# Kernel tuning notes

Hardware: AMD Instinct MI355X
Metric: run time of the kernel (lower is better)

Reference implementation:

```python
import jax, jax.numpy as jnp
import numpy as np

N = 50000
E = 100000
H = 768          # hidden_size
NH = 12          # num_heads
HD = H // NH     # head dim = 64
NG = 64          # number of graphs in batch
NC = 10          # num_classes
NEG_SLOPE = 0.2


def _p(key, shape, scale=0.05):
    return jax.random.normal(key, shape, dtype=jnp.float32) * scale


def setup_inputs() -> dict:
    key = jax.random.key(0)
    ks = jax.random.split(key, 24)
    x = jax.random.normal(ks[0], (N, 3), dtype=jnp.float32)
    edge_index = jax.random.randint(ks[1], (2, E), 0, N, dtype=jnp.int32)
    batch = jnp.sort(jax.random.randint(ks[2], (N,), 0, NG, dtype=jnp.int32))
    inp = {
        'x': x, 'edge_index': edge_index, 'batch': batch,
        # GCN layers
        'w1': _p(ks[3], (3, H)), 'b1': jnp.zeros((H,), jnp.float32),
        'w2': _p(ks[4], (H, H)), 'b2': jnp.zeros((H,), jnp.float32),
        'w3': _p(ks[5], (H, H)), 'b3': jnp.zeros((H,), jnp.float32),
        # GAT layer 1
        'wg1': _p(ks[6], (H, H)), 'as1': _p(ks[7], (NH, HD)), 'ad1': _p(ks[8], (NH, HD)), 'bg1': jnp.zeros((H,), jnp.float32),
        # GAT layer 2
        'wg2': _p(ks[9], (H, H)), 'as2': _p(ks[10], (NH, HD)), 'ad2': _p(ks[11], (NH, HD)), 'bg2': jnp.zeros((H,), jnp.float32),
        # classifier MLP
        'wc1': _p(ks[12], (H, H // 2)), 'bc1': jnp.zeros((H // 2,), jnp.float32),
        'wc2': _p(ks[13], (H // 2, NC)), 'bc2': jnp.zeros((NC,), jnp.float32),
    }
    return inp


def _add_self_loops(edge_index):
    loop = jnp.arange(N, dtype=edge_index.dtype)
    src = jnp.concatenate([edge_index[0], loop])
    dst = jnp.concatenate([edge_index[1], loop])
    return src, dst


def gcn_conv(x, w, b, src, dst):
    # PyG GCNConv: self-loops + symmetric normalization D^-1/2 A D^-1/2
    h = x @ w                                   # [N, out]
    deg = jnp.zeros((N,), h.dtype).at[dst].add(1.0)   # includes self-loops -> >= 1
    dinv = jax.lax.rsqrt(deg)
    norm = (dinv[src] * dinv[dst])[:, None]     # [E', 1]
    msg = h[src] * norm                          # gather-scale
    out = jnp.zeros_like(h).at[dst].add(msg)     # scatter-add
    return out + b


def gat_conv(x, w, a_src, a_dst, b, src, dst):
    # PyG GATConv: self-loops, LeakyReLU(0.2), scatter-softmax over dst, concat heads
    h = (x @ w).reshape(N, NH, HD)
    alpha_s = jnp.einsum('nhd,hd->nh', h, a_src)  # [N, H]
    alpha_d = jnp.einsum('nhd,hd->nh', h, a_dst)
    e = jax.nn.leaky_relu(alpha_s[src] + alpha_d[dst], NEG_SLOPE)  # [E', H]
    m = jax.ops.segment_max(e, dst, num_segments=N)                 # [N, H]
    ex = jnp.exp(e - m[dst])
    s = jax.ops.segment_sum(ex, dst, num_segments=N)
    alpha = ex / s[dst]                                             # [E', H]
    out = jax.ops.segment_sum(h[src] * alpha[:, :, None], dst, num_segments=N)
    return out.reshape(N, NH * HD) + b


def global_mean_pool(x, batch):
    s = jax.ops.segment_sum(x, batch, num_segments=NG)
    cnt = jax.ops.segment_sum(jnp.ones((N,), x.dtype), batch, num_segments=NG)
    return s / jnp.maximum(cnt, 1.0)[:, None]


def reference(x, edge_index, batch, w1, b1, w2, b2, w3, b3,
              wg1, as1, ad1, bg1, wg2, as2, ad2, bg2,
              wc1, bc1, wc2, bc2):
    src, dst = _add_self_loops(edge_index)
    h = jax.nn.relu(gcn_conv(x, w1, b1, src, dst))
    # dropout is identity in eval mode
    h = jax.nn.relu(gcn_conv(h, w2, b2, src, dst))
    h = jax.nn.relu(gcn_conv(h, w3, b3, src, dst))
    h = jax.nn.relu(gat_conv(h, wg1, as1, ad1, bg1, src, dst))
    h = gat_conv(h, wg2, as2, ad2, bg2, src, dst)
    g = global_mean_pool(h, batch)                 # [NG, H]
    z = jax.nn.relu(g @ wc1 + bc1)
    logits = z @ wc2 + bc2                         # [NG, NC]
    return logits
```

## Files before the change

### kernel.cpp

```cpp
#include <hip/hip_runtime.h>
#include <math.h>

#define N_NODES 50000
#define N_EDGES 100000
#define H 768
#define NH 12
#define HD 64
#define NG 64
#define NC 10
#define H2 384
#define PCH 32
#define NSB 196

typedef _Float16 h8  __attribute__((ext_vector_type(8)));
typedef _Float16 h4v __attribute__((ext_vector_type(4)));
typedef float    ffrag __attribute__((ext_vector_type(4)));

__device__ _Float16 g_ah[(size_t)N_NODES * H];
__device__ _Float16 g_ch[(size_t)N_NODES * H];
__device__ _Float16 g_wh[4 * H * H];
__device__ float    g_dinv[N_NODES];
__device__ int      g_degi[N_NODES];
__device__ int      g_bsum[256];
__device__ int      g_boff[256];
__device__ int      g_cursor[N_NODES];
__device__ int      g_rowptr[N_NODES + 1];
__device__ int      g_csrsrc[N_EDGES];
__device__ float    g_aS[(size_t)N_NODES * NH];
__device__ float    g_aD[(size_t)N_NODES * NH];
__device__ float    g_selfc[(size_t)N_NODES * NH];
__device__ float    g_coef[(size_t)N_EDGES * NH];
__device__ float    g_ppool[(size_t)NG * PCH * H];

__device__ inline int clampi(int v, int hi) { return (v < 0) ? 0 : (v >= hi ? hi - 1 : v); }

__device__ inline void gload_lds16(const _Float16* g, _Float16* s) {
    __builtin_amdgcn_global_load_lds(
        (const __attribute__((address_space(1))) void*)g,
        (__attribute__((address_space(3))) void*)s, 16, 0, 0);
}

__global__ void fill_i32(int* p, int n, int v) {
    int i = blockIdx.x * blockDim.x + threadIdx.x;
    if (i < n) p[i] = v;
}

__global__ void count_deg(const int* __restrict__ dst, int* __restrict__ degi) {
    int e = blockIdx.x * blockDim.x + threadIdx.x;
    if (e < N_EDGES) atomicAdd(&degi[clampi(dst[e], N_NODES)], 1);
}

__global__ __launch_bounds__(256) void scan1(const int* __restrict__ degi, int* __restrict__ bsum) {
    __shared__ int s[256];
    int b = blockIdx.x, t = threadIdx.x;
    int idx = b * 256 + t;
    s[t] = (idx < N_NODES) ? degi[idx] : 0;
    __syncthreads();
    for (int off = 128; off > 0; off >>= 1) {
        if (t < off) s[t] += s[t + off];
        __syncthreads();
    }
    if (t == 0) bsum[b] = s[0];
}

__global__ __launch_bounds__(256) void scan2(const int* __restrict__ bsum, int* __restrict__ boff,
                                             int* __restrict__ rowptr) {
    __shared__ int s[256];
    int t = threadIdx.x;
    int v = (t < NSB) ? bsum[t] : 0;
    s[t] = v;
    __syncthreads();
    for (int off = 1; off < 256; off <<= 1) {
        int x = (t >= off) ? s[t - off] : 0;
        __syncthreads();
        s[t] += x;
        __syncthreads();
    }
    if (t < NSB) boff[t] = s[t] - v;
    if (t == NSB - 1) rowptr[N_NODES] = s[t];
}

__global__ __launch_bounds__(256) void scan3(const int* __restrict__ degi, const int* __restrict__ boff,
                                             int* __restrict__ rowptr, int* __restrict__ cursor,
                                             float* __restrict__ dinv) {
    __shared__ int s[256];
    int b = blockIdx.x, t = threadIdx.x;
    int idx = b * 256 + t;
    int v = (idx < N_NODES) ? degi[idx] : 0;
    s[t] = v;
    __syncthreads();
    for (int off = 1; off < 256; off <<= 1) {
        int x = (t >= off) ? s[t - off] : 0;
        __syncthreads();
        s[t] += x;
        __syncthreads();
    }
    if (idx < N_NODES) {
        int excl = s[t] - v + boff[b];
        rowptr[idx] = excl;
        cursor[idx] = excl;
        dinv[idx] = rsqrtf((float)v + 1.0f);
    }
}

__global__ void bin_edges(const int* __restrict__ src, const int* __restrict__ dst,
                          int* __restrict__ cursor, int* __restrict__ csrsrc) {
    int e = blockIdx.x * blockDim.x + threadIdx.x;
    if (e >= N_EDGES) return;
    int d = clampi(dst[e], N_NODES);
    int pos = atomicAdd(&cursor[d], 1);
    if (pos >= 0 && pos < N_EDGES) csrsrc[pos] = clampi(src[e], N_NODES);
}

__global__ void split_wT4(const float* __restrict__ w2, const float* __restrict__ w3,
                          const float* __restrict__ wg1, const float* __restrict__ wg2,
                          _Float16* __restrict__ out) {
    int idx = blockIdx.x * blockDim.x + threadIdx.x;
    if (idx >= 4 * H * H) return;
    int l = idx / (H * H), r = idx % (H * H);
    const float* w = (l == 0) ? w2 : (l == 1) ? w3 : (l == 2) ? wg1 : wg2;
    int n = r % H, k = r / H;
    out[(size_t)l * H * H + (size_t)n * H + k] = (_Float16)w[(size_t)k * H + n];
}

__global__ void gcn1_fused(const int* __restrict__ rowptr, const int* __restrict__ csrsrc,
                           const float* __restrict__ x, const float* __restrict__ dinv,
                           const float* __restrict__ w1, const float* __restrict__ b1,
                           _Float16* __restrict__ hi) {
    int d = blockIdx.x * 2 + (threadIdx.x / 96);
    int t = threadIdx.x % 96;
    if (d >= N_NODES) return;
    float dd = dinv[d];
    float c = dd * dd;
    float s0 = x[d*3] * c, s1 = x[d*3+1] * c, s2 = x[d*3+2] * c;
    int beg = rowptr[d], end = rowptr[d + 1];
    for (int i = beg; i < end; i++) {
        int s = csrsrc[i];
        float cc = dinv[s] * dd;
        s0 += x[s*3] * cc; s1 += x[s*3+1] * cc; s2 += x[s*3+2] * cc;
    }
    int j0 = t * 8;
    h8 o;
    #pragma unroll
    for (int k = 0; k < 8; k++) {
        int j = j0 + k;
        float v = s0 * w1[j] + s1 * w1[H + j] + s2 * w1[2*H + j] + b1[j];
        o[k] = (_Float16)fmaxf(v, 0.f);
    }
    ((h8*)(hi + (size_t)d * H))[t] = o;
}

__global__ __launch_bounds__(512) void gemm_f16(const _Float16* __restrict__ a,
                                                const _Float16* __restrict__ bt,
                                                _Float16* __restrict__ C, int M,
                                                const float* __restrict__ asf,
                                                const float* __restrict__ adf,
                                                float* __restrict__ aS,
                                                float* __restrict__ aD) {
    __shared__ _Float16 sA[2][2][128 * 32], sB[2][2][128 * 32];
    int tid = threadIdx.x;
    int wave = tid >> 6, lane = tid & 63;
    int quad = lane >> 4, l16 = lane & 15;

    int id = blockIdx.x;
    int x = id & 7;
    int s = id >> 3;
    int strip = x + 8 * (s / 6);
    int colt = s % 6;
    if (strip >= (N_NODES + 127) / 128) return;
    int row0 = strip * 128, col0 = colt * 128;
    int wr = (wave >> 1) * 32, wc = (wave & 1) * 64;

    int rr = lane >> 2;
    int kc = (((lane & 3) ^ ((lane >> 3) & 3)) << 3);
    const _Float16* gptr[4];
    int sel[4];
    int soff[4];
    #pragma unroll
    for (int k = 0; k < 4; k++) {
        int sg = wave * 4 + k;
        int isA = (sg < 16);
        int s2 = sg & 15;
        int khalf = s2 >> 3, rowgroup = s2 & 7;
        int r = (isA ? row0 : col0) + rowgroup * 16 + rr;
        if (isA && r >= M) r = M - 1;
        gptr[k] = (isA ? a : bt) + (size_t)r * H + khalf * 32 + kc;
        sel[k] = isA ? 0 : 1;
        soff[k] = khalf * 4096 + rowgroup * 512;
    }

    int fsw = (quad ^ ((l16 >> 1) & 3)) * 8;

    ffrag acc[2][4];
    #pragma unroll
    for (int i = 0; i < 2; i++)
        #pragma unroll
        for (int j = 0; j < 4; j++) { ffrag z = {0.f, 0.f, 0.f, 0.f}; acc[i][j] = z; }

    #pragma unroll
    for (int k = 0; k < 4; k++)
        gload_lds16(gptr[k], (sel[k] ? &sB[0][0][0] : &sA[0][0][0]) + soff[k]);

    #pragma unroll 1
    for (int kt = 0; kt < H / 64; kt++) {
        int cur = kt & 1;
        __syncthreads();
        if (kt + 1 < H / 64) {
            int koff = (kt + 1) * 64;
            #pragma unroll
            for (int k = 0; k < 4; k++)
                gload_lds16(gptr[k] + koff,
                            (sel[k] ? &sB[cur ^ 1][0][0] : &sA[cur ^ 1][0][0]) + soff[k]);
        }

        #pragma unroll
        for (int kk = 0; kk < 2; kk++) {
            const _Float16* pA = sA[cur][kk];
            const _Float16* pB = sB[cur][kk];
            h8 fa[2], fb[4];
            #pragma unroll
            for (int i = 0; i < 2; i++)
                fa[i] = *reinterpret_cast<const h8*>(&pA[(wr + i * 16 + l16) * 32 + fsw]);
            #pragma unroll
            for (int j = 0; j < 4; j++)
                fb[j] = *reinterpret_cast<const h8*>(&pB[(wc + j * 16 + l16) * 32 + fsw]);
            #pragma unroll
            for (int i = 0; i < 2; i++)
                #pragma unroll
                for (int j = 0; j < 4; j++)
                    acc[i][j] = __builtin_amdgcn_mfma_f32_16x16x32_f16(fa[i], fb[j], acc[i][j], 0, 0, 0);
        }
    }

    #pragma unroll
    for (int i = 0; i < 2; i++)
        #pragma unroll
        for (int r = 0; r < 4; r++) {
            int row = row0 + wr + i * 16 + quad * 4 + r;
            if (row >= M) continue;
            #pragma unroll
            for (int j = 0; j < 4; j++)
                C[(size_t)row * H + col0 + wc + j * 16 + l16] = (_Float16)acc[i][j][r];
        }

    if (asf) {
        int head = (col0 + wc) >> 6;
        float as_c[4], ad_c[4];
        #pragma unroll
        for (int j = 0; j < 4; j++) {
            int col = col0 + wc + j * 16 + l16;
            as_c[j] = asf[col];
            ad_c[j] = adf[col];
        }
        #pragma unroll
        for (int i = 0; i < 2; i++)
            #pragma unroll
            for (int r = 0; r < 4; r++) {
                float ps = 0.f, pd = 0.f;
                #pragma unroll
                for (int j = 0; j < 4; j++) {
                    ps += acc[i][j][r] * as_c[j];
                    pd += acc[i][j][r] * ad_c[j];
                }
                ps += __shfl_xor(ps, 1);  pd += __shfl_xor(pd, 1);
                ps += __shfl_xor(ps, 2);  pd += __shfl_xor(pd, 2);
                ps += __shfl_xor(ps, 4);  pd += __shfl_xor(pd, 4);
                ps += __shfl_xor(ps, 8);  pd += __shfl_xor(pd, 8);
                int row = row0 + wr + i * 16 + quad * 4 + r;
                if (l16 == 0 && row < M) {
                    aS[row * NH + head] = ps;
                    aD[row * NH + head] = pd;
                }
            }
    }
}

__global__ void gcn_gather(const int* __restrict__ rowptr, const int* __restrict__ csrsrc,
                           const _Float16* __restrict__ h, const float* __restrict__ dinv,
                           const float* __restrict__ bias, _Float16* __restrict__ hi) {
    int d = blockIdx.x * 2 + (threadIdx.x / 96);
    int t = threadIdx.x % 96;
    if (d >= N_NODES) return;
    float dd = dinv[d];
    float c = dd * dd;
    h8 v = ((const h8*)(h + (size_t)d * H))[t];
    float acc[8];
    #pragma unroll
    for (int k = 0; k < 8; k++) acc[k] = (float)v[k] * c;
    int beg = rowptr[d], end = rowptr[d + 1];
    for (int i = beg; i < end; i++) {
        int s = csrsrc[i];
        float cc = dinv[s] * dd;
        h8 u = ((const h8*)(h + (size_t)s * H))[t];
        #pragma unroll
        for (int k = 0; k < 8; k++) acc[k] += (float)u[k] * cc;
    }
    float4 b0 = ((const float4*)bias)[2 * t];
    float4 b1 = ((const float4*)bias)[2 * t + 1];
    h8 o;
    o[0] = (_Float16)fmaxf(acc[0] + b0.x, 0.f);
    o[1] = (_Float16)fmaxf(acc[1] + b0.y, 0.f);
    o[2] = (_Float16)fmaxf(acc[2] + b0.z, 0.f);
    o[3] = (_Float16)fmaxf(acc[3] + b0.w, 0.f);
    o[4] = (_Float16)fmaxf(acc[4] + b1.x, 0.f);
    o[5] = (_Float16)fmaxf(acc[5] + b1.y, 0.f);
    o[6] = (_Float16)fmaxf(acc[6] + b1.z, 0.f);
    o[7] = (_Float16)fmaxf(acc[7] + b1.w, 0.f);
    ((h8*)(hi + (size_t)d * H))[t] = o;
}

__device__ inline float lrelu(float v) { return (v > 0.f) ? v : 0.2f * v; }

__global__ void gat_stats(const int* __restrict__ rowptr, const int* __restrict__ csrsrc,
                          const float* __restrict__ aS, const float* __restrict__ aD,
                          float* __restrict__ selfc, float* __restrict__ coef) {
    int idx = blockIdx.x * blockDim.x + threadIdx.x;
    if (idx >= N_NODES * NH) return;
    int d = idx / NH, hh = idx % NH;
    int beg = rowptr[d], end = rowptr[d + 1];
    float adv = aD[idx];
    float eself = lrelu(aS[idx] + adv);
    float m = eself;
    for (int i = beg; i < end; i++)
        m = fmaxf(m, lrelu(aS[csrsrc[i] * NH + hh] + adv));
    float ssum = __expf(eself - m);
    for (int i = beg; i < end; i++)
        ssum += __expf(lrelu(aS[csrsrc[i] * NH + hh] + adv) - m);
    float inv = 1.0f / ssum;
    selfc[idx] = __expf(eself - m) * inv;
    for (int i = beg; i < end; i++)
        coef[(size_t)i * NH + hh] = __expf(lrelu(aS[csrsrc[i] * NH + hh] + adv) - m) * inv;
}

__global__ void gat_gather(const int* __restrict__ rowptr, const int* __restrict__ csrsrc,
                           const _Float16* __restrict__ h, const float* __restrict__ selfc,
                           const float* __restrict__ coef, const float* __restrict__ bias,
                           _Float16* __restrict__ hi, int relu) {
    int d = blockIdx.x * 2 + (threadIdx.x / 96);
    int t = threadIdx.x % 96;
    if (d >= N_NODES) return;
    int hh = t >> 3;
    int beg = rowptr[d], end = rowptr[d + 1];
    float cself = selfc[d * NH + hh];
    h8 v = ((const h8*)(h + (size_t)d * H))[t];
    float acc[8];
    #pragma unroll
    for (int k = 0; k < 8; k++) acc[k] = (float)v[k] * cself;
    for (int i = beg; i < end; i++) {
        int s = csrsrc[i];
        float c = coef[(size_t)i * NH + hh];
        h8 u = ((const h8*)(h + (size_t)s * H))[t];
        #pragma unroll
        for (int k = 0; k < 8; k++) acc[k] += (float)u[k] * c;
    }
    float4 b0 = ((const float4*)bias)[2 * t];
    float4 b1 = ((const float4*)bias)[2 * t + 1];
    acc[0] += b0.x; acc[1] += b0.y; acc[2] += b0.z; acc[3] += b0.w;
    acc[4] += b1.x; acc[5] += b1.y; acc[6] += b1.z; acc[7] += b1.w;
    if (relu) {
        #pragma unroll
        for (int k = 0; k < 8; k++) acc[k] = fmaxf(acc[k], 0.f);
    }
    h8 o;
    #pragma unroll
    for (int k = 0; k < 8; k++) o[k] = (_Float16)acc[k];
    ((h8*)(hi + (size_t)d * H))[t] = o;
}

__device__ inline int lower_bound_i(const int* b, int n, int key) {
    int lo = 0, hi = n;
    while (lo < hi) { int mid = (lo + hi) >> 1; if (b[mid] < key) lo = mid + 1; else hi = mid; }
    return lo;
}

__global__ void pool_partial(const int* __restrict__ batch, const _Float16* __restrict__ h,
                             float* __restrict__ ppool) {
    int g = blockIdx.x / PCH, c = blockIdx.x % PCH;
    int t = threadIdx.x;
    int lo = lower_bound_i(batch, N_NODES, g);
    int hi = lower_bound_i(batch, N_NODES, g + 1);
    int len = hi - lo;
    int chunk = (len + PCH - 1) / PCH;
    int s = lo + c * chunk;
    int e = s + chunk; if (e > hi) e = hi;
    float4 a = {0, 0, 0, 0};
    for (int n = s; n < e; n++) {
        h4v v = ((const h4v*)(h + (size_t)n * H))[t];
        a.x += (float)v[0]; a.y += (float)v[1]; a.z += (float)v[2]; a.w += (float)v[3];
    }
    ((float4*)(ppool + (size_t)blockIdx.x * H))[t] = a;
}

__global__ __launch_bounds__(384) void pool_mlp(const int* __restrict__ batch,
                                                const float* __restrict__ ppool,
                                                const float* __restrict__ wc1,
                                                const float* __restrict__ bc1,
                                                const float* __restrict__ wc2,
                                                const float* __restrict__ bc2,
                                                float* __restrict__ out) {
    __shared__ float row[H];
    __shared__ float z[H2];
    int g = blockIdx.x, t = threadIdx.x;
    int lo = lower_bound_i(batch, N_NODES, g);
    int hi = lower_bound_i(batch, N_NODES, g + 1);
    float inv = 1.0f / fmaxf((float)(hi - lo), 1.0f);
    for (int c0 = t; c0 < H; c0 += 384) {
        float a = 0.f;
        for (int c = 0; c < PCH; c++) a += ppool[(size_t)(g * PCH + c) * H + c0];
        row[c0] = a * inv;
    }
    __syncthreads();
    float acc = bc1[t];
    for (int k = 0; k < H; k++) acc += row[k] * wc1[(size_t)k * H2 + t];
    z[t] = fmaxf(acc, 0.f);
    __syncthreads();
    if (t < NC) {
        float l = bc2[t];
        for (int k = 0; k < H2; k++) l += z[k] * wc2[(size_t)k * NC + t];
        out[g * NC + t] = l;
    }
}

extern "C" void kernel_launch(void* const* d_in, const int* in_sizes, int n_in,
                              void* d_out, int out_size, void* d_ws, size_t ws_size,
                              hipStream_t stream) {
    (void)d_ws; (void)ws_size;
    const float* x     = (const float*)d_in[0];
    const int*   ei    = (const int*)d_in[1];
    const int*   batch = (const int*)d_in[2];
    const float* w1  = (const float*)d_in[3];  const float* b1  = (const float*)d_in[4];
    const float* w2  = (const float*)d_in[5];  const float* b2  = (const float*)d_in[6];
    const float* w3  = (const float*)d_in[7];  const float* b3  = (const float*)d_in[8];
    const float* wg1 = (const float*)d_in[9];  const float* as1 = (const float*)d_in[10];
    const float* ad1 = (const float*)d_in[11]; const float* bg1 = (const float*)d_in[12];
    const float* wg2 = (const float*)d_in[13]; const float* as2 = (const float*)d_in[14];
    const float* ad2 = (const float*)d_in[15]; const float* bg2 = (const float*)d_in[16];
    const float* wc1 = (const float*)d_in[17]; const float* bc1 = (const float*)d_in[18];
    const float* wc2 = (const float*)d_in[19]; const float* bc2 = (const float*)d_in[20];

    const int* srcp = ei;
    const int* dstp = ei + N_EDGES;

    float *dinv, *aS, *aD, *selfc, *coef, *ppool;
    _Float16 *ah, *ch, *wh;
    int *degi, *bsum, *boff, *cursor, *rowptr, *csrsrc;
    hipGetSymbolAddress((void**)&ah,     HIP_SYMBOL(g_ah));
    hipGetSymbolAddress((void**)&ch,     HIP_SYMBOL(g_ch));
    hipGetSymbolAddress((void**)&wh,     HIP_SYMBOL(g_wh));
    hipGetSymbolAddress((void**)&dinv,   HIP_SYMBOL(g_dinv));
    hipGetSymbolAddress((void**)&degi,   HIP_SYMBOL(g_degi));
    hipGetSymbolAddress((void**)&bsum,   HIP_SYMBOL(g_bsum));
    hipGetSymbolAddress((void**)&boff,   HIP_SYMBOL(g_boff));
    hipGetSymbolAddress((void**)&cursor, HIP_SYMBOL(g_cursor));
    hipGetSymbolAddress((void**)&rowptr, HIP_SYMBOL(g_rowptr));
    hipGetSymbolAddress((void**)&csrsrc, HIP_SYMBOL(g_csrsrc));
    hipGetSymbolAddress((void**)&aS,     HIP_SYMBOL(g_aS));
    hipGetSymbolAddress((void**)&aD,     HIP_SYMBOL(g_aD));
    hipGetSymbolAddress((void**)&selfc,  HIP_SYMBOL(g_selfc));
    hipGetSymbolAddress((void**)&coef,   HIP_SYMBOL(g_coef));
    hipGetSymbolAddress((void**)&ppool,  HIP_SYMBOL(g_ppool));

    auto cdiv = [](int a, int b) { return (a + b - 1) / b; };
    int ggrid = 8 * cdiv(cdiv(N_NODES, 128), 8) * (H / 128);
    int ngath = cdiv(N_NODES, 2);
    size_t HH = (size_t)H * H;

    split_wT4<<<cdiv(4*H*H,256),256,0,stream>>>(w2, w3, wg1, wg2, wh);

    fill_i32<<<cdiv(N_NODES,256),256,0,stream>>>(degi, N_NODES, 0);
    count_deg<<<cdiv(N_EDGES,256),256,0,stream>>>(dstp, degi);
    scan1<<<NSB,256,0,stream>>>(degi, bsum);
    scan2<<<1,256,0,stream>>>(bsum, boff, rowptr);
    scan3<<<NSB,256,0,stream>>>(degi, boff, rowptr, cursor, dinv);
    bin_edges<<<cdiv(N_EDGES,256),256,0,stream>>>(srcp, dstp, cursor, csrsrc);

    gcn1_fused<<<ngath,192,0,stream>>>(rowptr, csrsrc, x, dinv, w1, b1, ah);

    gemm_f16<<<ggrid,512,0,stream>>>(ah, wh + 0*HH, ch, N_NODES,
                                     (const float*)nullptr, (const float*)nullptr,
                                     (float*)nullptr, (float*)nullptr);
    gcn_gather<<<ngath,192,0,stream>>>(rowptr, csrsrc, ch, dinv, b2, ah);

    gemm_f16<<<ggrid,512,0,stream>>>(ah, wh + 1*HH, ch, N_NODES,
                                     (const float*)nullptr, (const float*)nullptr,
                                     (float*)nullptr, (float*)nullptr);
    gcn_gather<<<ngath,192,0,stream>>>(rowptr, csrsrc, ch, dinv, b3, ah);

    gemm_f16<<<ggrid,512,0,stream>>>(ah, wh + 2*HH, ch, N_NODES, as1, ad1, aS, aD);
    gat_stats<<<cdiv(N_NODES*NH,256),256,0,stream>>>(rowptr, csrsrc, aS, aD, selfc, coef);
    gat_gather<<<ngath,192,0,stream>>>(rowptr, csrsrc, ch, selfc, coef, bg1, ah, 1);

    gemm_f16<<<ggrid,512,0,stream>>>(ah, wh + 3*HH, ch, N_NODES, as2, ad2, aS, aD);
    gat_stats<<<cdiv(N_NODES*NH,256),256,0,stream>>>(rowptr, csrsrc, aS, aD, selfc, coef);
    gat_gather<<<ngath,192,0,stream>>>(rowptr, csrsrc, ch, selfc, coef, bg2, ah, 0);

    pool_partial<<<NG*PCH,192,0,stream>>>(batch, ah, ppool);
    pool_mlp<<<NG,384,0,stream>>>(batch, ppool, wc1, bc1, wc2, bc2, (float*)d_out);
}
```

Baseline: 819.1 us.

## Enlarge GEMM tile to 256x128 with triple-buffered LDS pipeline and XCD remap

The f16 MFMA GEMM now uses a 256x128 output tile per block, so each wave computes 64x64 instead of 32x64. The K loop keeps three 64-wide LDS buffers and prefetches two steps ahead, with explicit vmcnt/lgkmcnt waits and raw barriers instead of __syncthreads. It raises MFMA priority during compute and remaps block ids round-robin over 8 groups of 147 (likely per-XCD). The aim is more reuse per loaded tile and better hiding of global load latency, at the cost of more accumulator registers and 144KB of LDS per block, which limits occupancy.

```diff
diff --git a/kernel.cpp b/kernel.cpp
--- a/kernel.cpp
+++ b/kernel.cpp
@@ -157,103 +157,151 @@
                                                 const float* __restrict__ adf,
                                                 float* __restrict__ aS,
                                                 float* __restrict__ aD) {
-    __shared__ _Float16 sA[2][2][128 * 32], sB[2][2][128 * 32];
+    __shared__ alignas(16) _Float16 lds[3][24576];
+
     int tid = threadIdx.x;
     int wave = tid >> 6, lane = tid & 63;
     int quad = lane >> 4, l16 = lane & 15;
-
-    int id = blockIdx.x;
-    int x = id & 7;
-    int s = id >> 3;
-    int strip = x + 8 * (s / 6);
-    int colt = s % 6;
-    if (strip >= (N_NODES + 127) / 128) return;
-    int row0 = strip * 128, col0 = colt * 128;
-    int wr = (wave >> 1) * 32, wc = (wave & 1) * 64;
-
-    int rr = lane >> 2;
-    int kc = (((lane & 3) ^ ((lane >> 3) & 3)) << 3);
-    const _Float16* gptr[4];
-    int sel[4];
-    int soff[4];
-    #pragma unroll
-    for (int k = 0; k < 4; k++) {
-        int sg = wave * 4 + k;
-        int isA = (sg < 16);
-        int s2 = sg & 15;
-        int khalf = s2 >> 3, rowgroup = s2 & 7;
-        int r = (isA ? row0 : col0) + rowgroup * 16 + rr;
-        if (isA && r >= M) r = M - 1;
-        gptr[k] = (isA ? a : bt) + (size_t)r * H + khalf * 32 + kc;
-        sel[k] = isA ? 0 : 1;
-        soff[k] = khalf * 4096 + rowgroup * 512;
-    }
-
-    int fsw = (quad ^ ((l16 >> 1) & 3)) * 8;
-
-    ffrag acc[2][4];
-    #pragma unroll
-    for (int i = 0; i < 2; i++)
+    int wm = wave >> 1, wn = wave & 1;
+
+    int orig = blockIdx.x;
+    int wgid = (orig & 7) * 147 + (orig >> 3);
+    int strip = wgid / 6, colt = wgid % 6;
+    int row0 = strip * 256, col0 = colt * 128;
+
+    int lr = lane >> 3;
+    int lc = lane & 7;
+    int cg = lc ^ lr;
+    const _Float16* gA[4];
+    const _Float16* gB[2];
+    int stA[4], stB[2];
+    #pragma unroll
+    for (int g = 0; g < 4; g++) {
+        int rA = row0 + wave * 32 + g * 8 + lr;
+        if (rA >= M) rA = M - 1;
+        gA[g] = a + (size_t)rA * H + cg * 8;
+        stA[g] = (wave * 32 + g * 8) * 64;
+    }
+    #pragma unroll
+    for (int g = 0; g < 2; g++) {
+        int rB = col0 + wave * 16 + g * 8 + lr;
+        gB[g] = bt + (size_t)rB * H + cg * 8;
+        stB[g] = 16384 + (wave * 16 + g * 8) * 64;
+    }
+
+    int swz = l16 & 7;
+    int offA[4][2], offB[4][2];
+    #pragma unroll
+    for (int i = 0; i < 4; i++)
+        #pragma unroll
+        for (int kk = 0; kk < 2; kk++) {
+            offA[i][kk] = (wm * 64 + i * 16 + l16) * 64 + (((kk * 4 + quad) ^ swz) * 8);
+            offB[i][kk] = 16384 + (wn * 64 + i * 16 + l16) * 64 + (((kk * 4 + quad) ^ swz) * 8);
+        }
+
+    ffrag acc[4][4];
+    #pragma unroll
+    for (int i = 0; i < 4; i++)
         #pragma unroll
         for (int j = 0; j < 4; j++) { ffrag z = {0.f, 0.f, 0.f, 0.f}; acc[i][j] = z; }
 
-    #pragma unroll
-    for (int k = 0; k < 4; k++)
-        gload_lds16(gptr[k], (sel[k] ? &sB[0][0][0] : &sA[0][0][0]) + soff[k]);
-
+    _Float16* p0 = &lds[0][0];
+    _Float16* p1 = &lds[1][0];
+    _Float16* p2 = &lds[2][0];
+
+    #pragma unroll
+    for (int g = 0; g < 4; g++) gload_lds16(gA[g], p0 + stA[g]);
+    #pragma unroll
+    for (int g = 0; g < 2; g++) gload_lds16(gB[g], p0 + stB[g]);
+    #pragma unroll
+    for (int g = 0; g < 4; g++) gload_lds16(gA[g] + 64, p1 + stA[g]);
+    #pragma unroll
+    for (int g = 0; g < 2; g++) gload_lds16(gB[g] + 64, p1 + stB[g]);
+    asm volatile("s_waitcnt vmcnt(6)" ::: "memory");
+    __builtin_amdgcn_s_barrier();
+    asm volatile("" ::: "memory");
+
+    _Float16 *pc = p0, *pn = p1, *pf = p2;
     #pragma unroll 1
     for (int kt = 0; kt < H / 64; kt++) {
-        int cur = kt & 1;
-        __syncthreads();
-        if (kt + 1 < H / 64) {
-            int koff = (kt + 1) * 64;
-            #pragma unroll
-            for (int k = 0; k < 4; k++)
-                gload_lds16(gptr[k] + koff,
-                            (sel[k] ? &sB[cur ^ 1][0][0] : &sA[cur ^ 1][0][0]) + soff[k]);
+        if (kt < H / 64 - 2) {
+            #pragma unroll
+            for (int g = 0; g < 4; g++) gload_lds16(gA[g] + (kt + 2) * 64, pf + stA[g]);
         }
-
-        #pragma unroll
-        for (int kk = 0; kk < 2; kk++) {
-            const _Float16* pA = sA[cur][kk];
-            const _Float16* pB = sB[cur][kk];
-            h8 fa[2], fb[4];
-            #pragma unroll
-            for (int i = 0; i < 2; i++)
-                fa[i] = *reinterpret_cast<const h8*>(&pA[(wr + i * 16 + l16) * 32 + fsw]);
-            #pragma unroll
-            for (int j = 0; j < 4; j++)
-                fb[j] = *reinterpret_cast<const h8*>(&pB[(wc + j * 16 + l16) * 32 + fsw]);
+        h8 fb[4][2], fa[2][2];
+        #pragma unroll
+        for (int j = 0; j < 4; j++)
+            #pragma unroll
+            for (int kk = 0; kk < 2; kk++)
+                fb[j][kk] = *reinterpret_cast<const h8*>(pc + offB[j][kk]);
+        #pragma unroll
+        for (int i = 0; i < 2; i++)
+            #pragma unroll
+            for (int kk = 0; kk < 2; kk++)
+                fa[i][kk] = *reinterpret_cast<const h8*>(pc + offA[i][kk]);
+        __builtin_amdgcn_s_setprio(1);
+        #pragma unroll
+        for (int kk = 0; kk < 2; kk++)
             #pragma unroll
             for (int i = 0; i < 2; i++)
                 #pragma unroll
                 for (int j = 0; j < 4; j++)
-                    acc[i][j] = __builtin_amdgcn_mfma_f32_16x16x32_f16(fa[i], fb[j], acc[i][j], 0, 0, 0);
+                    acc[i][j] = __builtin_amdgcn_mfma_f32_16x16x32_f16(fa[i][kk], fb[j][kk], acc[i][j], 0, 0, 0);
+        __builtin_amdgcn_s_setprio(0);
+        asm volatile("s_waitcnt lgkmcnt(0)" ::: "memory");
+        __builtin_amdgcn_sched_barrier(0);
+        __builtin_amdgcn_s_barrier();
+        asm volatile("" ::: "memory");
+        if (kt < H / 64 - 2) {
+            #pragma unroll
+            for (int g = 0; g < 2; g++) gload_lds16(gB[g] + (kt + 2) * 64, pf + stB[g]);
         }
-    }
-
-    #pragma unroll
-    for (int i = 0; i < 2; i++)
+        h8 fa2[2][2];
+        #pragma unroll
+        for (int i = 0; i < 2; i++)
+            #pragma unroll
+            for (int kk = 0; kk < 2; kk++)
+                fa2[i][kk] = *reinterpret_cast<const h8*>(pc + offA[2 + i][kk]);
+        __builtin_amdgcn_s_setprio(1);
+        #pragma unroll
+        for (int kk = 0; kk < 2; kk++)
+            #pragma unroll
+            for (int i = 0; i < 2; i++)
+                #pragma unroll
+                for (int j = 0; j < 4; j++)
+                    acc[2 + i][j] = __builtin_amdgcn_mfma_f32_16x16x32_f16(fa2[i][kk], fb[j][kk], acc[2 + i][j], 0, 0, 0);
+        __builtin_amdgcn_s_setprio(0);
+        asm volatile("s_waitcnt lgkmcnt(0)" ::: "memory");
+        __builtin_amdgcn_sched_barrier(0);
+        if (kt < H / 64 - 2) asm volatile("s_waitcnt vmcnt(6)" ::: "memory");
+        else                 asm volatile("s_waitcnt vmcnt(0)" ::: "memory");
+        __builtin_amdgcn_s_barrier();
+        asm volatile("" ::: "memory");
+        _Float16* t = pc; pc = pn; pn = pf; pf = t;
+    }
+
+    #pragma unroll
+    for (int i = 0; i < 4; i++)
         #pragma unroll
         for (int r = 0; r < 4; r++) {
-            int row = row0 + wr + i * 16 + quad * 4 + r;
+            int row = row0 + wm * 64 + i * 16 + quad * 4 + r;
             if (row >= M) continue;
             #pragma unroll
             for (int j = 0; j < 4; j++)
-                C[(size_t)row * H + col0 + wc + j * 16 + l16] = (_Float16)acc[i][j][r];
+                C[(size_t)row * H + col0 + wn * 64 + j * 16 + l16] = (_Float16)acc[i][j][r];
         }
 
     if (asf) {
-        int head = (col0 + wc) >> 6;
+        int head = (col0 + wn * 64) >> 6;
         float as_c[4], ad_c[4];
         #pragma unroll
         for (int j = 0; j < 4; j++) {
-            int col = col0 + wc + j * 16 + l16;
+            int col = col0 + wn * 64 + j * 16 + l16;
             as_c[j] = asf[col];
             ad_c[j] = adf[col];
         }
         #pragma unroll
-        for (int i = 0; i < 2; i++)
+        for (int i = 0; i < 4; i++)
             #pragma unroll
             for (int r = 0; r < 4; r++) {
                 float ps = 0.f, pd = 0.f;
@@ -266,7 +314,7 @@
                 ps += __shfl_xor(ps, 2);  pd += __shfl_xor(pd, 2);
                 ps += __shfl_xor(ps, 4);  pd += __shfl_xor(pd, 4);
                 ps += __shfl_xor(ps, 8);  pd += __shfl_xor(pd, 8);
-                int row = row0 + wr + i * 16 + quad * 4 + r;
+                int row = row0 + wm * 64 + i * 16 + quad * 4 + r;
                 if (l16 == 0 && row < M) {
                     aS[row * NH + head] = ps;
                     aD[row * NH + head] = pd;
@@ -461,7 +509,7 @@
     hipGetSymbolAddress((void**)&ppool,  HIP_SYMBOL(g_ppool));
 
     auto cdiv = [](int a, int b) { return (a + b - 1) / b; };
-    int ggrid = 8 * cdiv(cdiv(N_NODES, 128), 8) * (H / 128);
+    int ggrid = cdiv(N_NODES, 256) * (H / 128);
     int ngath = cdiv(N_NODES, 2);
     size_t HH = (size_t)H * H;
 
```

Result: slower. 858.0 us (+4.7%).

## Make GEMM persistent with register-resident weight slices and 4-stage A pipeline

Applied to the files above, without the earlier changes.

The f16 GEMM becomes a persistent kernel with 1024-thread blocks. Each block owns a 256-column slice and keeps its B (weight) fragments in registers for the whole K dimension, then walks 4–5 consecutive 128-row strips, streaming only A through a 4-buffer LDS ring with cross-strip prefetch. This removes the repeated B reloads and the per-tile launch overhead of the old 128x128 tiling. The cost is very high register pressure (48 h8 fragments per lane), which can cause spills or low occupancy. The attention-dot epilogue now reduces across waves through shared memory.

```diff
diff --git a/kernel.cpp b/kernel.cpp
--- a/kernel.cpp
+++ b/kernel.cpp
@@ -11,6 +11,7 @@
 #define H2 384
 #define PCH 32
 #define NSB 196
+#define GBLK 85
 
 typedef _Float16 h8  __attribute__((ext_vector_type(8)));
 typedef _Float16 h4v __attribute__((ext_vector_type(4)));
@@ -150,128 +151,155 @@
     ((h8*)(hi + (size_t)d * H))[t] = o;
 }
 
-__global__ __launch_bounds__(512) void gemm_f16(const _Float16* __restrict__ a,
-                                                const _Float16* __restrict__ bt,
-                                                _Float16* __restrict__ C, int M,
-                                                const float* __restrict__ asf,
-                                                const float* __restrict__ adf,
-                                                float* __restrict__ aS,
-                                                float* __restrict__ aD) {
-    __shared__ _Float16 sA[2][2][128 * 32], sB[2][2][128 * 32];
+__global__ __launch_bounds__(1024, 4) void gemm_f16(const _Float16* __restrict__ a,
+                                                    const _Float16* __restrict__ bt,
+                                                    _Float16* __restrict__ C, int M,
+                                                    const float* __restrict__ asf,
+                                                    const float* __restrict__ adf,
+                                                    float* __restrict__ aS,
+                                                    float* __restrict__ aD) {
+    __shared__ alignas(16) _Float16 As[4][8192];
+    __shared__ float alsS[16][64];
+    __shared__ float alsD[16][64];
+
     int tid = threadIdx.x;
     int wave = tid >> 6, lane = tid & 63;
     int quad = lane >> 4, l16 = lane & 15;
-
-    int id = blockIdx.x;
-    int x = id & 7;
-    int s = id >> 3;
-    int strip = x + 8 * (s / 6);
-    int colt = s % 6;
-    if (strip >= (N_NODES + 127) / 128) return;
-    int row0 = strip * 128, col0 = colt * 128;
-    int wr = (wave >> 1) * 32, wc = (wave & 1) * 64;
-
-    int rr = lane >> 2;
-    int kc = (((lane & 3) ^ ((lane >> 3) & 3)) << 3);
-    const _Float16* gptr[4];
-    int sel[4];
-    int soff[4];
+    int wm = wave >> 3, wn = wave & 7;
+
+    int colgrp = blockIdx.x / GBLK;
+    int b      = blockIdx.x % GBLK;
+    int cnt = (b < 51) ? 5 : 4;
+    int s0  = b * 4 + (b < 51 ? b : 51);
+    int col0 = colgrp * 256;
+    int cw   = col0 + wn * 32;
+
+    h8 bf0[24], bf1[24];
+    {
+        const _Float16* b0p = bt + (size_t)(cw + l16) * H + quad * 8;
+        const _Float16* b1p = bt + (size_t)(cw + 16 + l16) * H + quad * 8;
+        #pragma unroll
+        for (int ks = 0; ks < 24; ks++) {
+            bf0[ks] = *reinterpret_cast<const h8*>(b0p + ks * 32);
+            bf1[ks] = *reinterpret_cast<const h8*>(b1p + ks * 32);
+        }
+    }
+
+    int lr = lane >> 3;
+    int cg = (lane & 7) ^ lr;
+    int stoff = wave * 8 * 64;
+    int arow  = wave * 8 + lr;
+    int swz = l16 & 7;
+    int offA[4][2];
     #pragma unroll
-    for (int k = 0; k < 4; k++) {
-        int sg = wave * 4 + k;
-        int isA = (sg < 16);
-        int s2 = sg & 15;
-        int khalf = s2 >> 3, rowgroup = s2 & 7;
-        int r = (isA ? row0 : col0) + rowgroup * 16 + rr;
-        if (isA && r >= M) r = M - 1;
-        gptr[k] = (isA ? a : bt) + (size_t)r * H + khalf * 32 + kc;
-        sel[k] = isA ? 0 : 1;
-        soff[k] = khalf * 4096 + rowgroup * 512;
-    }
-
-    int fsw = (quad ^ ((l16 >> 1) & 3)) * 8;
-
-    ffrag acc[2][4];
+    for (int i = 0; i < 4; i++)
+        #pragma unroll
+        for (int kk = 0; kk < 2; kk++)
+            offA[i][kk] = (wm * 64 + i * 16 + l16) * 64 + (((kk * 4 + quad) ^ swz) * 8);
+
+    float asc0 = 0.f, asc1 = 0.f, adc0 = 0.f, adc1 = 0.f;
+    if (asf) {
+        asc0 = asf[cw + l16];      asc1 = asf[cw + 16 + l16];
+        adc0 = adf[cw + l16];      adc1 = adf[cw + 16 + l16];
+    }
+
+    ffrag acc[4][2];
     #pragma unroll
-    for (int i = 0; i < 2; i++)
-        #pragma unroll
-        for (int j = 0; j < 4; j++) { ffrag z = {0.f, 0.f, 0.f, 0.f}; acc[i][j] = z; }
-
-    #pragma unroll
-    for (int k = 0; k < 4; k++)
-        gload_lds16(gptr[k], (sel[k] ? &sB[0][0][0] : &sA[0][0][0]) + soff[k]);
-
+    for (int i = 0; i < 4; i++)
+        #pragma unroll
+        for (int j = 0; j < 2; j++) { ffrag z = {0.f, 0.f, 0.f, 0.f}; acc[i][j] = z; }
+
+    {
+        int r = s0 * 128 + arow; if (r >= M) r = M - 1;
+        const _Float16* ap = a + (size_t)r * H + cg * 8;
+        gload_lds16(ap,        &As[0][0] + stoff);
+        gload_lds16(ap + 64,   &As[1][0] + stoff);
+        gload_lds16(ap + 128,  &As[2][0] + stoff);
+    }
+    asm volatile("s_waitcnt vmcnt(2)" ::: "memory");
+    __builtin_amdgcn_s_barrier();
+
+    int row0 = s0 * 128;
     #pragma unroll 1
-    for (int kt = 0; kt < H / 64; kt++) {
-        int cur = kt & 1;
-        __syncthreads();
-        if (kt + 1 < H / 64) {
-            int koff = (kt + 1) * 64;
+    for (int sdx = 0; sdx < cnt; sdx++) {
+        #pragma unroll
+        for (int kt = 0; kt < 12; kt++) {
+            {
+                int prow = row0 + ((kt >= 9) ? 128 : 0) + arow;
+                if (prow >= M) prow = M - 1;
+                int pkk = (kt >= 9) ? (kt - 9) : (kt + 3);
+                gload_lds16(a + (size_t)prow * H + pkk * 64 + cg * 8,
+                            &As[(kt + 3) & 3][0] + stoff);
+            }
+            const _Float16* pc = &As[kt & 3][0];
+            h8 fa[4][2];
             #pragma unroll
-            for (int k = 0; k < 4; k++)
-                gload_lds16(gptr[k] + koff,
-                            (sel[k] ? &sB[cur ^ 1][0][0] : &sA[cur ^ 1][0][0]) + soff[k]);
+            for (int i = 0; i < 4; i++)
+                #pragma unroll
+                for (int kk = 0; kk < 2; kk++)
+                    fa[i][kk] = *reinterpret_cast<const h8*>(pc + offA[i][kk]);
+            asm volatile("s_waitcnt lgkmcnt(0)" ::: "memory");
+            __builtin_amdgcn_sched_barrier(0);
+            __builtin_amdgcn_s_setprio(1);
+            #pragma unroll
+            for (int kk = 0; kk < 2; kk++)
+                #pragma unroll
+                for (int i = 0; i < 4; i++) {
+                    acc[i][0] = __builtin_amdgcn_mfma_f32_16x16x32_f16(fa[i][kk], bf0[kt * 2 + kk], acc[i][0], 0, 0, 0);
+                    acc[i][1] = __builtin_amdgcn_mfma_f32_16x16x32_f16(fa[i][kk], bf1[kt * 2 + kk], acc[i][1], 0, 0, 0);
+                }
+            __builtin_amdgcn_s_setprio(0);
+            asm volatile("s_waitcnt vmcnt(2)" ::: "memory");
+            __builtin_amdgcn_sched_barrier(0);
+            __builtin_amdgcn_s_barrier();
         }
 
         #pragma unroll
-        for (int kk = 0; kk < 2; kk++) {
-            const _Float16* pA = sA[cur][kk];
-            const _Float16* pB = sB[cur][kk];
-            h8 fa[2], fb[4];
-            #pragma unroll
-            for (int i = 0; i < 2; i++)
-                fa[i] = *reinterpret_cast<const h8*>(&pA[(wr + i * 16 + l16) * 32 + fsw]);
-            #pragma unroll
-            for (int j = 0; j < 4; j++)
-                fb[j] = *reinterpret_cast<const h8*>(&pB[(wc + j * 16 + l16) * 32 + fsw]);
-            #pragma unroll
-            for (int i = 0; i < 2; i++)
-                #pragma unroll
-                for (int j = 0; j < 4; j++)
-                    acc[i][j] = __builtin_amdgcn_mfma_f32_16x16x32_f16(fa[i], fb[j], acc[i][j], 0, 0, 0);
-        }
-    }
-
-    #pragma unroll
-    for (int i = 0; i < 2; i++)
-        #pragma unroll
-        for (int r = 0; r < 4; r++) {
-            int row = row0 + wr + i * 16 + quad * 4 + r;
-            if (row >= M) continue;
-            #pragma unroll
-            for (int j = 0; j < 4; j++)
-                C[(size_t)row * H + col0 + wc + j * 16 + l16] = (_Float16)acc[i][j][r];
-        }
-
-    if (asf) {
-        int head = (col0 + wc) >> 6;
-        float as_c[4], ad_c[4];
-        #pragma unroll
-        for (int j = 0; j < 4; j++) {
-            int col = col0 + wc + j * 16 + l16;
-            as_c[j] = asf[col];
-            ad_c[j] = adf[col];
-        }
-        #pragma unroll
-        for (int i = 0; i < 2; i++)
+        for (int i = 0; i < 4; i++)
             #pragma unroll
             for (int r = 0; r < 4; r++) {
-                float ps = 0.f, pd = 0.f;
-                #pragma unroll
-                for (int j = 0; j < 4; j++) {
-                    ps += acc[i][j][r] * as_c[j];
-                    pd += acc[i][j][r] * ad_c[j];
-                }
-                ps += __shfl_xor(ps, 1);  pd += __shfl_xor(pd, 1);
-                ps += __shfl_xor(ps, 2);  pd += __shfl_xor(pd, 2);
-                ps += __shfl_xor(ps, 4);  pd += __shfl_xor(pd, 4);
-                ps += __shfl_xor(ps, 8);  pd += __shfl_xor(pd, 8);
-                int row = row0 + wr + i * 16 + quad * 4 + r;
-                if (l16 == 0 && row < M) {
-                    aS[row * NH + head] = ps;
-                    aD[row * NH + head] = pd;
+                int row = row0 + wm * 64 + i * 16 + quad * 4 + r;
+                if (row < M) {
+                    C[(size_t)row * H + cw + l16]      = (_Float16)acc[i][0][r];
+                    C[(size_t)row * H + cw + 16 + l16] = (_Float16)acc[i][1][r];
                 }
             }
+
+        if (asf) {
+            #pragma unroll
+            for (int i = 0; i < 4; i++)
+                #pragma unroll
+                for (int r = 0; r < 4; r++) {
+                    float ps = acc[i][0][r] * asc0 + acc[i][1][r] * asc1;
+                    float pd = acc[i][0][r] * adc0 + acc[i][1][r] * adc1;
+                    ps += __shfl_xor(ps, 1);  pd += __shfl_xor(pd, 1);
+                    ps += __shfl_xor(ps, 2);  pd += __shfl_xor(pd, 2);
+                    ps += __shfl_xor(ps, 4);  pd += __shfl_xor(pd, 4);
+                    ps += __shfl_xor(ps, 8);  pd += __shfl_xor(pd, 8);
+                    if (l16 == 0) {
+                        alsS[wave][i * 16 + quad * 4 + r] = ps;
+                        alsD[wave][i * 16 + quad * 4 + r] = pd;
+                    }
+                }
+            __syncthreads();
+            if ((wn & 1) == 0) {
+                float s = alsS[wave][lane] + alsS[wave + 1][lane];
+                float d = alsD[wave][lane] + alsD[wave + 1][lane];
+                int row = row0 + wm * 64 + lane;
+                int head = colgrp * 4 + (wn >> 1);
+                if (row < M) {
+                    aS[row * NH + head] = s;
+                    aD[row * NH + head] = d;
+                }
+            }
+            __syncthreads();
+        }
+
+        #pragma unroll
+        for (int i = 0; i < 4; i++)
+            #pragma unroll
+            for (int j = 0; j < 2; j++) { ffrag z = {0.f, 0.f, 0.f, 0.f}; acc[i][j] = z; }
+        row0 += 128;
     }
 }
 
@@ -461,7 +489,7 @@
     hipGetSymbolAddress((void**)&ppool,  HIP_SYMBOL(g_ppool));
 
     auto cdiv = [](int a, int b) { return (a + b - 1) / b; };
-    int ggrid = 8 * cdiv(cdiv(N_NODES, 128), 8) * (H / 128);
+    int ggrid = 3 * GBLK;
     int ngath = cdiv(N_NODES, 2);
     size_t HH = (size_t)H * H;
 
@@ -476,21 +504,21 @@
 
     gcn1_fused<<<ngath,192,0,stream>>>(rowptr, csrsrc, x, dinv, w1, b1, ah);
 
-    gemm_f16<<<ggrid,512,0,stream>>>(ah, wh + 0*HH, ch, N_NODES,
-                                     (const float*)nullptr, (const float*)nullptr,
-                                     (float*)nullptr, (float*)nullptr);
+    gemm_f16<<<ggrid,1024,0,stream>>>(ah, wh + 0*HH, ch, N_NODES,
+                                      (const float*)nullptr, (const float*)nullptr,
+                                      (float*)nullptr, (float*)nullptr);
     gcn_gather<<<ngath,192,0,stream>>>(rowptr, csrsrc, ch, dinv, b2, ah);
 
-    gemm_f16<<<ggrid,512,0,stream>>>(ah, wh + 1*HH, ch, N_NODES,
-                                     (const float*)nullptr, (const float*)nullptr,
-                                     (float*)nullptr, (float*)nullptr);
+    gemm_f16<<<ggrid,1024,0,stream>>>(ah, wh + 1*HH, ch, N_NODES,
+                                      (const float*)nullptr, (const float*)nullptr,
+                                      (float*)nullptr, (float*)nullptr);
     gcn_gather<<<ngath,192,0,stream>>>(rowptr, csrsrc, ch, dinv, b3, ah);
 
-    gemm_f16<<<ggrid,512,0,stream>>>(ah, wh + 2*HH, ch, N_NODES, as1, ad1, aS, aD);
+    gemm_f16<<<ggrid,1024,0,stream>>>(ah, wh + 2*HH, ch, N_NODES, as1, ad1, aS, aD);
     gat_stats<<<cdiv(N_NODES*NH,256),256,0,stream>>>(rowptr, csrsrc, aS, aD, selfc, coef);
     gat_gather<<<ngath,192,0,stream>>>(rowptr, csrsrc, ch, selfc, coef, bg1, ah, 1);
 
-    gemm_f16<<<ggrid,512,0,stream>>>(ah, wh + 3*HH, ch, N_NODES, as2, ad2, aS, aD);
+    gemm_f16<<<ggrid,1024,0,stream>>>(ah, wh + 3*HH, ch, N_NODES, as2, ad2, aS, aD);
     gat_stats<<<cdiv(N_NODES*NH,256),256,0,stream>>>(rowptr, csrsrc, aS, aD, selfc, coef);
     gat_gather<<<ngath,192,0,stream>>>(rowptr, csrsrc, ch, selfc, coef, bg2, ah, 0);
 
```

Result: slower. 1.543 ms (+88.3%).

## Fuse GAT softmax stats into gather and shrink GEMM K-tile to 32

Applied to the files above, without the earlier changes.

Removes the separate gat_stats kernel and its selfc/coef buffers. The gather kernel now computes the per-destination softmax max, sum and coefficients inline, which cuts two launches and the coefficient write/read traffic but repeats the exp and aS lookups in each of the 8 threads sharing a head. Separately, the GEMM's K-step per LDS stage drops from 64 to 32. That halves shared memory and global loads per stage but doubles the barrier and loop iterations.

```diff
diff --git a/kernel.cpp b/kernel.cpp
--- a/kernel.cpp
+++ b/kernel.cpp
@@ -28,8 +28,6 @@
 __device__ int      g_csrsrc[N_EDGES];
 __device__ float    g_aS[(size_t)N_NODES * NH];
 __device__ float    g_aD[(size_t)N_NODES * NH];
-__device__ float    g_selfc[(size_t)N_NODES * NH];
-__device__ float    g_coef[(size_t)N_EDGES * NH];
 __device__ float    g_ppool[(size_t)NG * PCH * H];
 
 __device__ inline int clampi(int v, int hi) { return (v < 0) ? 0 : (v >= hi ? hi - 1 : v); }
@@ -157,7 +155,7 @@
                                                 const float* __restrict__ adf,
                                                 float* __restrict__ aS,
                                                 float* __restrict__ aD) {
-    __shared__ _Float16 sA[2][2][128 * 32], sB[2][2][128 * 32];
+    __shared__ _Float16 sA[2][128 * 32], sB[2][128 * 32];
     int tid = threadIdx.x;
     int wave = tid >> 6, lane = tid & 63;
     int quad = lane >> 4, l16 = lane & 15;
@@ -173,20 +171,19 @@
 
     int rr = lane >> 2;
     int kc = (((lane & 3) ^ ((lane >> 3) & 3)) << 3);
-    const _Float16* gptr[4];
-    int sel[4];
-    int soff[4];
-    #pragma unroll
-    for (int k = 0; k < 4; k++) {
-        int sg = wave * 4 + k;
-        int isA = (sg < 16);
-        int s2 = sg & 15;
-        int khalf = s2 >> 3, rowgroup = s2 & 7;
+    const _Float16* gptr[2];
+    int sel[2];
+    int soff[2];
+    #pragma unroll
+    for (int k = 0; k < 2; k++) {
+        int sg = wave * 2 + k;
+        int isA = (sg < 8);
+        int rowgroup = sg & 7;
         int r = (isA ? row0 : col0) + rowgroup * 16 + rr;
         if (isA && r >= M) r = M - 1;
-        gptr[k] = (isA ? a : bt) + (size_t)r * H + khalf * 32 + kc;
+        gptr[k] = (isA ? a : bt) + (size_t)r * H + kc;
         sel[k] = isA ? 0 : 1;
-        soff[k] = khalf * 4096 + rowgroup * 512;
+        soff[k] = rowgroup * 512;
     }
 
     int fsw = (quad ^ ((l16 >> 1) & 3)) * 8;
@@ -198,38 +195,35 @@
         for (int j = 0; j < 4; j++) { ffrag z = {0.f, 0.f, 0.f, 0.f}; acc[i][j] = z; }
 
     #pragma unroll
-    for (int k = 0; k < 4; k++)
-        gload_lds16(gptr[k], (sel[k] ? &sB[0][0][0] : &sA[0][0][0]) + soff[k]);
+    for (int k = 0; k < 2; k++)
+        gload_lds16(gptr[k], (sel[k] ? &sB[0][0] : &sA[0][0]) + soff[k]);
 
     #pragma unroll 1
-    for (int kt = 0; kt < H / 64; kt++) {
+    for (int kt = 0; kt < H / 32; kt++) {
         int cur = kt & 1;
         __syncthreads();
-        if (kt + 1 < H / 64) {
-            int koff = (kt + 1) * 64;
+        if (kt + 1 < H / 32) {
+            int koff = (kt + 1) * 32;
             #pragma unroll
-            for (int k = 0; k < 4; k++)
+            for (int k = 0; k < 2; k++)
                 gload_lds16(gptr[k] + koff,
-                            (sel[k] ? &sB[cur ^ 1][0][0] : &sA[cur ^ 1][0][0]) + soff[k]);
+                            (sel[k] ? &sB[cur ^ 1][0] : &sA[cur ^ 1][0]) + soff[k]);
         }
 
-        #pragma unroll
-        for (int kk = 0; kk < 2; kk++) {
-            const _Float16* pA = sA[cur][kk];
-            const _Float16* pB = sB[cur][kk];
-            h8 fa[2], fb[4];
-            #pragma unroll
-            for (int i = 0; i < 2; i++)
-                fa[i] = *reinterpret_cast<const h8*>(&pA[(wr + i * 16 + l16) * 32 + fsw]);
+        const _Float16* pA = sA[cur];
+        const _Float16* pB = sB[cur];
+        h8 fa[2], fb[4];
+        #pragma unroll
+        for (int i = 0; i < 2; i++)
+            fa[i] = *reinterpret_cast<const h8*>(&pA[(wr + i * 16 + l16) * 32 + fsw]);
+        #pragma unroll
+        for (int j = 0; j < 4; j++)
+            fb[j] = *reinterpret_cast<const h8*>(&pB[(wc + j * 16 + l16) * 32 + fsw]);
+        #pragma unroll
+        for (int i = 0; i < 2; i++)
             #pragma unroll
             for (int j = 0; j < 4; j++)
-                fb[j] = *reinterpret_cast<const h8*>(&pB[(wc + j * 16 + l16) * 32 + fsw]);
-            #pragma unroll
-            for (int i = 0; i < 2; i++)
-                #pragma unroll
-                for (int j = 0; j < 4; j++)
-                    acc[i][j] = __builtin_amdgcn_mfma_f32_16x16x32_f16(fa[i], fb[j], acc[i][j], 0, 0, 0);
-        }
+                acc[i][j] = __builtin_amdgcn_mfma_f32_16x16x32_f16(fa[i], fb[j], acc[i][j], 0, 0, 0);
     }
 
     #pragma unroll
@@ -311,15 +305,17 @@
 
 __device__ inline float lrelu(float v) { return (v > 0.f) ? v : 0.2f * v; }
 
-__global__ void gat_stats(const int* __restrict__ rowptr, const int* __restrict__ csrsrc,
-                          const float* __restrict__ aS, const float* __restrict__ aD,
-                          float* __restrict__ selfc, float* __restrict__ coef) {
-    int idx = blockIdx.x * blockDim.x + threadIdx.x;
-    if (idx >= N_NODES * NH) return;
-    int d = idx / NH, hh = idx % NH;
+__global__ void gat_gather(const int* __restrict__ rowptr, const int* __restrict__ csrsrc,
+                           const _Float16* __restrict__ h, const float* __restrict__ aS,
+                           const float* __restrict__ aD, const float* __restrict__ bias,
+                           _Float16* __restrict__ hi, int relu) {
+    int d = blockIdx.x * 2 + (threadIdx.x / 96);
+    int t = threadIdx.x % 96;
+    if (d >= N_NODES) return;
+    int hh = t >> 3;
     int beg = rowptr[d], end = rowptr[d + 1];
-    float adv = aD[idx];
-    float eself = lrelu(aS[idx] + adv);
+    float adv = aD[d * NH + hh];
+    float eself = lrelu(aS[d * NH + hh] + adv);
     float m = eself;
     for (int i = beg; i < end; i++)
         m = fmaxf(m, lrelu(aS[csrsrc[i] * NH + hh] + adv));
@@ -327,28 +323,14 @@
     for (int i = beg; i < end; i++)
         ssum += __expf(lrelu(aS[csrsrc[i] * NH + hh] + adv) - m);
     float inv = 1.0f / ssum;
-    selfc[idx] = __expf(eself - m) * inv;
-    for (int i = beg; i < end; i++)
-        coef[(size_t)i * NH + hh] = __expf(lrelu(aS[csrsrc[i] * NH + hh] + adv) - m) * inv;
-}
-
-__global__ void gat_gather(const int* __restrict__ rowptr, const int* __restrict__ csrsrc,
-                           const _Float16* __restrict__ h, const float* __restrict__ selfc,
-                           const float* __restrict__ coef, const float* __restrict__ bias,
-                           _Float16* __restrict__ hi, int relu) {
-    int d = blockIdx.x * 2 + (threadIdx.x / 96);
-    int t = threadIdx.x % 96;
-    if (d >= N_NODES) return;
-    int hh = t >> 3;
-    int beg = rowptr[d], end = rowptr[d + 1];
-    float cself = selfc[d * NH + hh];
+    float cself = __expf(eself - m) * inv;
     h8 v = ((const h8*)(h + (size_t)d * H))[t];
     float acc[8];
     #pragma unroll
     for (int k = 0; k < 8; k++) acc[k] = (float)v[k] * cself;
     for (int i = beg; i < end; i++) {
         int s = csrsrc[i];
-        float c = coef[(size_t)i * NH + hh];
+        float c = __expf(lrelu(aS[s * NH + hh] + adv) - m) * inv;
         h8 u = ((const h8*)(h + (size_t)s * H))[t];
         #pragma unroll
         for (int k = 0; k < 8; k++) acc[k] += (float)u[k] * c;
@@ -441,7 +423,7 @@
     const int* srcp = ei;
     const int* dstp = ei + N_EDGES;
 
-    float *dinv, *aS, *aD, *selfc, *coef, *ppool;
+    float *dinv, *aS, *aD, *ppool;
     _Float16 *ah, *ch, *wh;
     int *degi, *bsum, *boff, *cursor, *rowptr, *csrsrc;
     hipGetSymbolAddress((void**)&ah,     HIP_SYMBOL(g_ah));
@@ -456,8 +438,6 @@
     hipGetSymbolAddress((void**)&csrsrc, HIP_SYMBOL(g_csrsrc));
     hipGetSymbolAddress((void**)&aS,     HIP_SYMBOL(g_aS));
     hipGetSymbolAddress((void**)&aD,     HIP_SYMBOL(g_aD));
-    hipGetSymbolAddress((void**)&selfc,  HIP_SYMBOL(g_selfc));
-    hipGetSymbolAddress((void**)&coef,   HIP_SYMBOL(g_coef));
     hipGetSymbolAddress((void**)&ppool,  HIP_SYMBOL(g_ppool));
 
     auto cdiv = [](int a, int b) { return (a + b - 1) / b; };
@@ -487,12 +467,10 @@
     gcn_gather<<<ngath,192,0,stream>>>(rowptr, csrsrc, ch, dinv, b3, ah);
 
     gemm_f16<<<ggrid,512,0,stream>>>(ah, wh + 2*HH, ch, N_NODES, as1, ad1, aS, aD);
-    gat_stats<<<cdiv(N_NODES*NH,256),256,0,stream>>>(rowptr, csrsrc, aS, aD, selfc, coef);
-    gat_gather<<<ngath,192,0,stream>>>(rowptr, csrsrc, ch, selfc, coef, bg1, ah, 1);
+    gat_gather<<<ngath,192,0,stream>>>(rowptr, csrsrc, ch, aS, aD, bg1, ah, 1);
 
     gemm_f16<<<ggrid,512,0,stream>>>(ah, wh + 3*HH, ch, N_NODES, as2, ad2, aS, aD);
-    gat_stats<<<cdiv(N_NODES*NH,256),256,0,stream>>>(rowptr, csrsrc, aS, aD, selfc, coef);
-    gat_gather<<<ngath,192,0,stream>>>(rowptr, csrsrc, ch, selfc, coef, bg2, ah, 0);
+    gat_gather<<<ngath,192,0,stream>>>(rowptr, csrsrc, ch, aS, aD, bg2, ah, 0);
 
     pool_partial<<<NG*PCH,192,0,stream>>>(batch, ah, ppool);
     pool_mlp<<<NG,384,0,stream>>>(batch, ppool, wc1, bc1, wc2, bc2, (float*)d_out);
```

After: 913.1 us. 11.5% more time.
